# Performance work log

Hardware: AMD Instinct MI355X
Metric: run time of the kernel (lower is better)

## Reference

```python
import jax, jax.numpy as jnp
import numpy as np

N, E, B = 50000, 800000, 64
NODE_DIM, EDGE_DIM, HID, H, L = 8, 16, 128, 4, 3
C = HID // H  # head dim = 32
NUM_CLASSES, NAV_DIM = 6, 4


def _layernorm(x, g, b, eps=1e-5):
    mu = x.mean(-1, keepdims=True)
    var = ((x - mu) ** 2).mean(-1, keepdims=True)
    return (x - mu) * jax.lax.rsqrt(var + eps) * g + b


def _gat_layer(x, src, dst, e_attr, W, We, a_s, a_d, a_e, bias, n):
    # x: [N,HID]; e_attr: [Etot,EDGE_DIM]; W: [HID,HID]; We: [EDGE_DIM,HID]
    xh = (x @ W).reshape(n, H, C)                      # [N,H,C]
    eh = (e_attr @ We).reshape(-1, H, C)               # [Etot,H,C]
    a_src = (xh * a_s).sum(-1)                         # [N,H]
    a_dst = (xh * a_d).sum(-1)                         # [N,H]
    alpha = a_src[src] + a_dst[dst] + (eh * a_e).sum(-1)  # [Etot,H]
    alpha = jax.nn.leaky_relu(alpha, 0.2)
    amax = jax.ops.segment_max(alpha, dst, num_segments=n)
    alpha = jnp.exp(alpha - amax[dst])
    denom = jax.ops.segment_sum(alpha, dst, num_segments=n)
    alpha = alpha / (denom[dst] + 1e-16)               # scatter-softmax over dst
    msg = xh[src] * alpha[:, :, None]                  # [Etot,H,C]
    out = jax.ops.segment_sum(msg, dst, num_segments=n)
    return out.reshape(n, HID) + bias


def setup_inputs():
    key = jax.random.key(0)
    ks = jax.random.split(key, 32)
    s = 0.05
    inp = {
        'x': jax.random.normal(ks[0], (N, NODE_DIM), jnp.float32),
        'edge_index': jax.random.randint(ks[1], (2, E), 0, N, jnp.int64),
        'edge_attr': jax.random.normal(ks[2], (E, EDGE_DIM), jnp.float32),
        'batch': jnp.sort(jax.random.randint(ks[3], (N,), 0, B, jnp.int64)),
        'proj_W': jax.random.normal(ks[4], (NODE_DIM, HID)) * s,
        'proj_b': jnp.zeros((HID,)),
        'lin_W': jax.random.normal(ks[5], (L, HID, HID)) * s,
        'lin_edge_W': jax.random.normal(ks[6], (L, EDGE_DIM, HID)) * s,
        'att_src': jax.random.normal(ks[7], (L, H, C)) * s,
        'att_dst': jax.random.normal(ks[8], (L, H, C)) * s,
        'att_edge': jax.random.normal(ks[9], (L, H, C)) * s,
        'conv_bias': jnp.zeros((L, HID)),
        'ln_g': jnp.ones((L, HID)),
        'ln_b': jnp.zeros((L, HID)),
        'sc_W1': jax.random.normal(ks[10], (HID, HID // 2)) * s,
        'sc_b1': jnp.zeros((HID // 2,)),
        'sc_W2': jax.random.normal(ks[11], (HID // 2, NUM_CLASSES)) * s,
        'sc_b2': jnp.zeros((NUM_CLASSES,)),
        'nav_W1': jax.random.normal(ks[12], (HID, HID // 2)) * s,
        'nav_b1': jnp.zeros((HID // 2,)),
        'nav_W2': jax.random.normal(ks[13], (HID // 2, NAV_DIM)) * s,
        'nav_b2': jnp.zeros((NAV_DIM,)),
    }
    return inp


def reference(x, edge_index, edge_attr, batch, proj_W, proj_b, lin_W, lin_edge_W,
              att_src, att_dst, att_edge, conv_bias, ln_g, ln_b,
              sc_W1, sc_b1, sc_W2, sc_b2, nav_W1, nav_b1, nav_W2, nav_b2):
    n = x.shape[0]
    h = jax.nn.relu(x @ proj_W + proj_b)
    # PyG GATConv default add_self_loops=True, edge_attr fill_value='mean'
    loops = jnp.arange(n)
    src = jnp.concatenate([edge_index[0], loops])
    dst = jnp.concatenate([edge_index[1], loops])
    ea = jnp.concatenate(
        [edge_attr, jnp.broadcast_to(edge_attr.mean(0), (n, edge_attr.shape[1]))], 0)
    for l in range(L):
        res = h
        h = _gat_layer(h, src, dst, ea, lin_W[l], lin_edge_W[l],
                       att_src[l], att_dst[l], att_edge[l], conv_bias[l], n)
        h = _layernorm(h + res, ln_g[l], ln_b[l])
        h = jax.nn.relu(h)
        # dropout is identity in eval / p=0
    counts = jax.ops.segment_sum(jnp.ones((n,), h.dtype), batch, num_segments=B)
    graph = jax.ops.segment_sum(h, batch, num_segments=B) / jnp.maximum(counts, 1.0)[:, None]
    scene = jax.nn.relu(graph @ sc_W1 + sc_b1) @ sc_W2 + sc_b2
    nav = jax.nn.sigmoid(jax.nn.relu(graph @ nav_W1 + nav_b1) @ nav_W2 + nav_b2)
    return (h, scene, nav, graph)
```

## Files before the change

kernel.cpp:

```cpp
#include <hip/hip_runtime.h>
#include <hip/hip_bf16.h>

constexpr int NN   = 50000;
constexpr int NE   = 800000;
constexpr int ETOT = NE + NN;
constexpr int BGR  = 64;
constexpr int HID  = 128;
constexpr int HEADS= 4;
constexpr int CDIM = 32;
constexpr int EDIM = 16;
constexpr int NDIM = 8;
constexpr int LAYERS = 3;
constexpr int HALF = 64;
constexpr int NCLS = 6;
constexpr int NAVD = 4;

constexpr int OUT_SCENE = NN * HID;
constexpr int OUT_NAV   = OUT_SCENE + BGR*NCLS;
constexpr int OUT_GRAPH = OUT_NAV + BGR*NAVD;

__global__ void mean_ea_kernel(const float* __restrict__ ea, float* __restrict__ mean_sum) {
    __shared__ float sdata[256];
    int tid = threadIdx.x;
    float acc = 0.f;
    int stride = gridDim.x * blockDim.x;
    for (int i = blockIdx.x * blockDim.x + tid; i < NE * EDIM; i += stride)
        acc += ea[i];
    sdata[tid] = acc;
    __syncthreads();
    for (int off = 128; off >= 16; off >>= 1) {
        if (tid < off) sdata[tid] += sdata[tid + off];
        __syncthreads();
    }
    if (tid < 16) atomicAdd(&mean_sum[tid], sdata[tid]);
}

__global__ void precompute_kernel(const float* __restrict__ lin_edge_W,
                                  const float* __restrict__ att_edge,
                                  const float* __restrict__ mean_sum,
                                  float* __restrict__ w_e, float* __restrict__ mean_alpha) {
    int l = blockIdx.x;
    int t = threadIdx.x;
    __shared__ float we_s[EDIM * HEADS];
    const float* We = lin_edge_W + l * EDIM * HID;
    const float* ae = att_edge   + l * HEADS * CDIM;
    if (t < EDIM) {
        #pragma unroll
        for (int h = 0; h < HEADS; h++) {
            float s = 0.f;
            #pragma unroll
            for (int c = 0; c < CDIM; c++)
                s += We[t * HID + h * CDIM + c] * ae[h * CDIM + c];
            we_s[t * HEADS + h] = s;
            w_e[(l * EDIM + t) * HEADS + h] = s;
        }
    }
    __syncthreads();
    if (t < HEADS) {
        float s = 0.f;
        #pragma unroll
        for (int k = 0; k < EDIM; k++)
            s += (mean_sum[k] * (1.f / (float)NE)) * we_s[k * HEADS + t];
        mean_alpha[l * HEADS + t] = s;
    }
}

__global__ void proj_kernel(const float* __restrict__ x, const float* __restrict__ pW,
                            const float* __restrict__ pb, float* __restrict__ h) {
    int node = blockIdx.x;
    int t = threadIdx.x;
    __shared__ float xr[NDIM];
    if (t < NDIM) xr[t] = x[node * NDIM + t];
    __syncthreads();
    float acc = pb[t];
    #pragma unroll
    for (int k = 0; k < NDIM; k++) acc += xr[k] * pW[k * HID + t];
    h[node * HID + t] = fmaxf(acc, 0.f);
}

__launch_bounds__(256, 2)
__global__ void xh_kernel(const float* __restrict__ hin, const float* __restrict__ W,
                          const float* __restrict__ As, const float* __restrict__ Ad,
                          float* __restrict__ xh, float* __restrict__ asrc,
                          float* __restrict__ adst) {
    __shared__ float Ws[HID * HID];
    {
        const float4* Wv = (const float4*)W;
        float4* Wsv = (float4*)Ws;
        #pragma unroll
        for (int i = 0; i < (HID * HID / 4) / 256; i++)
            Wsv[i * 256 + threadIdx.x] = Wv[i * 256 + threadIdx.x];
    }
    __syncthreads();
    int t = threadIdx.x;
    int c = t & 127;
    int lane = t & 63;
    int which = __builtin_amdgcn_readfirstlane(t >> 7);
    float myAs = As[c], myAd = Ad[c];
    int head = c >> 5;

    for (int base = blockIdx.x * 4; base < NN; base += gridDim.x * 4) {
        int n0 = base + which * 2;
        int n1 = n0 + 1;
        const float* __restrict__ h0 = hin + (size_t)n0 * HID;
        const float* __restrict__ h1 = hin + (size_t)n1 * HID;
        float a0e = 0.f, a0o = 0.f, a1e = 0.f, a1o = 0.f;
        #pragma unroll 8
        for (int k = 0; k < HID; k += 2) {
            float w0 = Ws[k * HID + c];
            float w1 = Ws[(k + 1) * HID + c];
            float h0e = h0[k], h0o = h0[k + 1];
            float h1e = h1[k], h1o = h1[k + 1];
            a0e = fmaf(h0e, w0, a0e);
            a0o = fmaf(h0o, w1, a0o);
            a1e = fmaf(h1e, w0, a1e);
            a1o = fmaf(h1o, w1, a1o);
        }
        float acc0 = a0e + a0o;
        float acc1 = a1e + a1o;
        xh[(size_t)n0 * HID + c] = acc0;
        xh[(size_t)n1 * HID + c] = acc1;
        float rs0 = acc0 * myAs, rd0 = acc0 * myAd;
        float rs1 = acc1 * myAs, rd1 = acc1 * myAd;
        #pragma unroll
        for (int off = 16; off > 0; off >>= 1) {
            rs0 += __shfl_xor(rs0, off);
            rd0 += __shfl_xor(rd0, off);
            rs1 += __shfl_xor(rs1, off);
            rd1 += __shfl_xor(rd1, off);
        }
        if ((lane & 31) == 0) {
            asrc[n0 * HEADS + head] = rs0;
            adst[n0 * HEADS + head] = rd0;
            asrc[n1 * HEADS + head] = rs1;
            adst[n1 * HEADS + head] = rd1;
        }
    }
}

__global__ void hist_kernel(const int* __restrict__ ei, int* __restrict__ counts) {
    int e = blockIdx.x * blockDim.x + threadIdx.x;
    if (e >= ETOT) return;
    int d = (e < NE) ? ei[NE + e] : (e - NE);
    atomicAdd(&counts[d], 1);
}

__global__ void scan_kernel(const int* __restrict__ counts, int* __restrict__ offsets) {
    __shared__ int wsum[16];
    __shared__ int carry_s;
    int lane = threadIdx.x & 63;
    int wid  = threadIdx.x >> 6;
    if (threadIdx.x == 0) carry_s = 0;
    __syncthreads();
    for (int base = 0; base < NN; base += 1024) {
        int i = base + threadIdx.x;
        int v = (i < NN) ? counts[i] : 0;
        int x = v;
        #pragma unroll
        for (int off = 1; off < 64; off <<= 1) {
            int y = __shfl_up(x, off);
            if (lane >= off) x += y;
        }
        if (lane == 63) wsum[wid] = x;
        __syncthreads();
        if (wid == 0) {
            int w = (lane < 16) ? wsum[lane] : 0;
            #pragma unroll
            for (int off = 1; off < 16; off <<= 1) {
                int y = __shfl_up(w, off);
                if (lane >= off) w += y;
            }
            if (lane < 16) wsum[lane] = w;
        }
        __syncthreads();
        int waveoff = (wid == 0) ? 0 : wsum[wid - 1];
        int carry = carry_s;
        if (i < NN) offsets[i] = carry + waveoff + x - v;
        __syncthreads();
        if (threadIdx.x == 0) carry_s = carry + wsum[15];
        __syncthreads();
    }
}

__global__ void scatter_kernel(const int* __restrict__ ei, const int* __restrict__ offsets,
                               int* __restrict__ fill, int* __restrict__ epos,
                               int* __restrict__ src_p) {
    int e = blockIdx.x * blockDim.x + threadIdx.x;
    if (e >= ETOT) return;
    int s, d;
    if (e < NE) { s = ei[e]; d = ei[NE + e]; }
    else        { s = d = e - NE; }
    int pos = offsets[d] + atomicAdd(&fill[d], 1);
    epos[e]   = pos;
    src_p[pos] = s;
}

__global__ void eterm_kernel(const float* __restrict__ ea,
                             const float* __restrict__ w_e, const float* __restrict__ mean_alpha,
                             const int* __restrict__ epos, float* __restrict__ dst, int nl) {
    __shared__ float we_s[LAYERS * EDIM * HEADS];
    __shared__ float ma_s[LAYERS * HEADS];
    if (threadIdx.x < nl * EDIM * HEADS) we_s[threadIdx.x] = w_e[threadIdx.x];
    if (threadIdx.x < nl * HEADS) ma_s[threadIdx.x] = mean_alpha[threadIdx.x];
    __syncthreads();
    int e = blockIdx.x * blockDim.x + threadIdx.x;
    if (e >= ETOT) return;
    int pos = epos[e];
    if (e < NE) {
        float er[EDIM];
        const float4* ev = (const float4*)(ea + (size_t)e * EDIM);
        float4 v0 = ev[0], v1 = ev[1], v2 = ev[2], v3 = ev[3];
        er[0]=v0.x; er[1]=v0.y; er[2]=v0.z; er[3]=v0.w;
        er[4]=v1.x; er[5]=v1.y; er[6]=v1.z; er[7]=v1.w;
        er[8]=v2.x; er[9]=v2.y; er[10]=v2.z; er[11]=v2.w;
        er[12]=v3.x; er[13]=v3.y; er[14]=v3.z; er[15]=v3.w;
        for (int l = 0; l < nl; l++) {
            float e0 = 0.f, e1 = 0.f, e2 = 0.f, e3 = 0.f;
            const float* ws = we_s + l * EDIM * HEADS;
            #pragma unroll
            for (int k = 0; k < EDIM; k++) {
                float xv = er[k];
                e0 += xv * ws[k * HEADS + 0];
                e1 += xv * ws[k * HEADS + 1];
                e2 += xv * ws[k * HEADS + 2];
                e3 += xv * ws[k * HEADS + 3];
            }
            *(float4*)(dst + (size_t)l * ETOT * HEADS + (size_t)pos * HEADS)
                = make_float4(e0, e1, e2, e3);
        }
    } else {
        for (int l = 0; l < nl; l++) {
            *(float4*)(dst + (size_t)l * ETOT * HEADS + (size_t)pos * HEADS)
                = make_float4(ma_s[l*HEADS+0], ma_s[l*HEADS+1], ma_s[l*HEADS+2], ma_s[l*HEADS+3]);
        }
    }
}

__launch_bounds__(256)
__global__ void aggregate_kernel(const int* __restrict__ src_p, const int* __restrict__ offsets,
                                 const int* __restrict__ counts,
                                 const float* __restrict__ eterm,
                                 const float* __restrict__ asrc, const float* __restrict__ adst,
                                 const float* __restrict__ xh,
                                 const float* __restrict__ hres, const float* __restrict__ bias,
                                 const float* __restrict__ lng, const float* __restrict__ lnb,
                                 float* __restrict__ hout) {
    int wid  = threadIdx.x >> 6;
    int lane = threadIdx.x & 63;
    int node = blockIdx.x * 4 + wid;
    if (node >= NN) return;
    int start = offsets[node];
    int deg   = counts[node];
    int head  = lane >> 4;
    int c0    = lane * 2;
    float ad_h = adst[node * HEADS + head];

    float m = -1e30f, dsum = 0.f, acc0 = 0.f, acc1 = 0.f;
    int j = 0;
    for (; j + 3 < deg; j += 4) {
        int p0 = start + j, p1 = p0 + 1, p2 = p0 + 2, p3 = p0 + 3;
        int s0 = src_p[p0], s1 = src_p[p1], s2 = src_p[p2], s3 = src_p[p3];
        float a0 = asrc[s0 * HEADS + head] + ad_h + eterm[(size_t)p0 * HEADS + head];
        float a1 = asrc[s1 * HEADS + head] + ad_h + eterm[(size_t)p1 * HEADS + head];
        float a2 = asrc[s2 * HEADS + head] + ad_h + eterm[(size_t)p2 * HEADS + head];
        float a3 = asrc[s3 * HEADS + head] + ad_h + eterm[(size_t)p3 * HEADS + head];
        a0 = (a0 > 0.f) ? a0 : 0.2f * a0;
        a1 = (a1 > 0.f) ? a1 : 0.2f * a1;
        a2 = (a2 > 0.f) ? a2 : 0.2f * a2;
        a3 = (a3 > 0.f) ? a3 : 0.2f * a3;
        float2 v0 = *(const float2*)(xh + (size_t)s0 * HID + c0);
        float2 v1 = *(const float2*)(xh + (size_t)s1 * HID + c0);
        float2 v2 = *(const float2*)(xh + (size_t)s2 * HID + c0);
        float2 v3 = *(const float2*)(xh + (size_t)s3 * HID + c0);
        float mn = fmaxf(m, fmaxf(fmaxf(a0, a1), fmaxf(a2, a3)));
        float sc = __expf(m - mn);
        float q0 = __expf(a0 - mn), q1 = __expf(a1 - mn);
        float q2 = __expf(a2 - mn), q3 = __expf(a3 - mn);
        dsum = fmaf(dsum, sc, (q0 + q1) + (q2 + q3));
        acc0 = fmaf(acc0, sc, fmaf(q0, v0.x, fmaf(q1, v1.x, fmaf(q2, v2.x, q3 * v3.x))));
        acc1 = fmaf(acc1, sc, fmaf(q0, v0.y, fmaf(q1, v1.y, fmaf(q2, v2.y, q3 * v3.y))));
        m = mn;
    }
    for (; j < deg; j++) {
        int pi = start + j;
        int s0 = src_p[pi];
        float a0 = asrc[s0 * HEADS + head] + ad_h + eterm[(size_t)pi * HEADS + head];
        a0 = (a0 > 0.f) ? a0 : 0.2f * a0;
        float2 v0 = *(const float2*)(xh + (size_t)s0 * HID + c0);
        float mn = fmaxf(m, a0);
        float sc = __expf(m - mn);
        float q0 = __expf(a0 - mn);
        dsum = fmaf(dsum, sc, q0);
        acc0 = fmaf(acc0, sc, q0 * v0.x);
        acc1 = fmaf(acc1, sc, q0 * v0.y);
        m = mn;
    }
    float inv = 1.f / (dsum + 1e-16f);
    float2 r = *(const float2*)(hres + (size_t)node * HID + c0);
    float v0 = acc0 * inv + bias[c0]     + r.x;
    float v1 = acc1 * inv + bias[c0 + 1] + r.y;

    float ssum = v0 + v1;
    #pragma unroll
    for (int off = 32; off > 0; off >>= 1) ssum += __shfl_xor(ssum, off);
    float mu = ssum * (1.f / 128.f);
    float d0 = v0 - mu, d1 = v1 - mu;
    float vs = d0 * d0 + d1 * d1;
    #pragma unroll
    for (int off = 32; off > 0; off >>= 1) vs += __shfl_xor(vs, off);
    float rstd = rsqrtf(vs * (1.f / 128.f) + 1e-5f);
    float y0 = fmaxf(d0 * rstd * lng[c0]     + lnb[c0],     0.f);
    float y1 = fmaxf(d1 * rstd * lng[c0 + 1] + lnb[c0 + 1], 0.f);
    *(float2*)(hout + (size_t)node * HID + c0) = make_float2(y0, y1);
}

__launch_bounds__(512)
__global__ void head_kernel(const float* __restrict__ h, const int* __restrict__ batch,
                            const float* __restrict__ scW1, const float* __restrict__ scb1,
                            const float* __restrict__ scW2, const float* __restrict__ scb2,
                            const float* __restrict__ nvW1, const float* __restrict__ nvb1,
                            const float* __restrict__ nvW2, const float* __restrict__ nvb2,
                            float* __restrict__ out) {
    int b = blockIdx.x;
    int t = threadIdx.x;
    __shared__ float part[4][HID];
    __shared__ float gr[HID];
    __shared__ float h1[HALF];
    __shared__ float h2[HALF];
    int lo = 0, hi = NN;
    while (lo < hi) { int mid = (lo + hi) >> 1; if (batch[mid] < b) lo = mid + 1; else hi = mid; }
    int s0 = lo;
    lo = s0; hi = NN;
    while (lo < hi) { int mid = (lo + hi) >> 1; if (batch[mid] < b + 1) lo = mid + 1; else hi = mid; }
    int e0 = lo;
    int cnt = e0 - s0;

    int r  = t >> 7;
    int ch = t & 127;
    float acc = 0.f;
    for (int i = s0 + r; i < e0; i += 4) acc += h[(size_t)i * HID + ch];
    part[r][ch] = acc;
    __syncthreads();
    if (t < HID) {
        float g = (part[0][t] + part[1][t] + part[2][t] + part[3][t]) / fmaxf((float)cnt, 1.f);
        gr[t] = g;
        out[OUT_GRAPH + b * HID + t] = g;
    }
    __syncthreads();
    if (t < HALF) {
        float a = scb1[t], n = nvb1[t];
        #pragma unroll 4
        for (int k = 0; k < HID; k++) {
            float g = gr[k];
            a += g * scW1[k * HALF + t];
            n += g * nvW1[k * HALF + t];
        }
        h1[t] = fmaxf(a, 0.f);
        h2[t] = fmaxf(n, 0.f);
    }
    __syncthreads();
    if (t < NCLS) {
        float a = scb2[t];
        #pragma unroll 8
        for (int j = 0; j < HALF; j++) a += h1[j] * scW2[j * NCLS + t];
        out[OUT_SCENE + b * NCLS + t] = a;
    }
    if (t >= 64 && t < 64 + NAVD) {
        int q = t - 64;
        float a = nvb2[q];
        #pragma unroll 8
        for (int j = 0; j < HALF; j++) a += h2[j] * nvW2[j * NAVD + q];
        out[OUT_NAV + b * NAVD + q] = 1.f / (1.f + expf(-a));
    }
}

extern "C" void kernel_launch(void* const* d_in, const int* in_sizes, int n_in,
                              void* d_out, int out_size, void* d_ws, size_t ws_size,
                              hipStream_t stream) {
    const float* x        = (const float*)d_in[0];
    const int*   ei       = (const int*)  d_in[1];
    const float* ea       = (const float*)d_in[2];
    const int*   batch    = (const int*)  d_in[3];
    const float* proj_W   = (const float*)d_in[4];
    const float* proj_b   = (const float*)d_in[5];
    const float* lin_W    = (const float*)d_in[6];
    const float* lin_eW   = (const float*)d_in[7];
    const float* att_src  = (const float*)d_in[8];
    const float* att_dst  = (const float*)d_in[9];
    const float* att_edge = (const float*)d_in[10];
    const float* conv_bias= (const float*)d_in[11];
    const float* ln_g     = (const float*)d_in[12];
    const float* ln_b     = (const float*)d_in[13];
    const float* sc_W1    = (const float*)d_in[14];
    const float* sc_b1    = (const float*)d_in[15];
    const float* sc_W2    = (const float*)d_in[16];
    const float* sc_b2    = (const float*)d_in[17];
    const float* nav_W1   = (const float*)d_in[18];
    const float* nav_b1   = (const float*)d_in[19];
    const float* nav_W2   = (const float*)d_in[20];
    const float* nav_b2   = (const float*)d_in[21];
    float* out = (float*)d_out;

    char* w = (char*)d_ws;
    size_t off = 0;
    auto alloc = [&](size_t bytes) -> char* {
        char* p = w + off;
        off = (off + bytes + 255) & ~(size_t)255;
        return p;
    };
    size_t fixed = (size_t)NN*HID*4*2 + (size_t)NN*HEADS*4*2 + (size_t)NN*4*3
                 + (size_t)ETOT*4*2 + 16384;
    bool multi = (ws_size >= fixed + (size_t)LAYERS * ETOT * HEADS * 4 + 65536);
    int nl = multi ? LAYERS : 1;

    float* hA      = (float*)alloc((size_t)NN * HID * 4);
    float* xh      = (float*)alloc((size_t)NN * HID * 4);
    float* asrc    = (float*)alloc((size_t)NN * HEADS * 4);
    float* adst    = (float*)alloc((size_t)NN * HEADS * 4);
    int*   counts  = (int*)  alloc((size_t)NN * 4);
    int*   offsets = (int*)  alloc((size_t)NN * 4);
    int*   fill    = (int*)  alloc((size_t)NN * 4);
    int*   epos    = (int*)  alloc((size_t)ETOT * 4);
    int*   src_p   = (int*)  alloc((size_t)ETOT * 4);
    float* w_e     = (float*)alloc((size_t)LAYERS * EDIM * HEADS * 4);
    float* mean_s  = (float*)alloc(EDIM * 4);
    float* mean_al = (float*)alloc(LAYERS * HEADS * 4);
    float* eterm   = (float*)alloc((size_t)nl * ETOT * HEADS * 4);

    hipMemsetAsync(mean_s, 0, EDIM * 4, stream);
    hipMemsetAsync(counts, 0, (size_t)NN * 4, stream);
    hipMemsetAsync(fill,   0, (size_t)NN * 4, stream);

    mean_ea_kernel<<<256, 256, 0, stream>>>(ea, mean_s);
    precompute_kernel<<<LAYERS, 64, 0, stream>>>(lin_eW, att_edge, mean_s, w_e, mean_al);
    proj_kernel<<<NN, HID, 0, stream>>>(x, proj_W, proj_b, hA);

    int eblocks = (ETOT + 255) / 256;
    hist_kernel<<<eblocks, 256, 0, stream>>>(ei, counts);
    scan_kernel<<<1, 1024, 0, stream>>>(counts, offsets);
    scatter_kernel<<<eblocks, 256, 0, stream>>>(ei, offsets, fill, epos, src_p);
    if (multi)
        eterm_kernel<<<eblocks, 256, 0, stream>>>(ea, w_e, mean_al, epos, eterm, LAYERS);

    const float* hin = hA;
    float* hout = out;
    for (int l = 0; l < LAYERS; l++) {
        xh_kernel<<<512, 256, 0, stream>>>(hin, lin_W + (size_t)l * HID * HID,
                                           att_src + (size_t)l * HID,
                                           att_dst + (size_t)l * HID,
                                           xh, asrc, adst);
        if (!multi)
            eterm_kernel<<<eblocks, 256, 0, stream>>>(ea, w_e + (size_t)l * EDIM * HEADS,
                                                      mean_al + (size_t)l * HEADS,
                                                      epos, eterm, 1);
        const float* et_l = multi ? (eterm + (size_t)l * ETOT * HEADS) : eterm;
        aggregate_kernel<<<(NN + 3) / 4, 256, 0, stream>>>(src_p, offsets, counts,
                                                           et_l, asrc, adst, xh, hin,
                                                           conv_bias + (size_t)l * HID,
                                                           ln_g + (size_t)l * HID,
                                                           ln_b + (size_t)l * HID, hout);
        const float* tmp = hin;
        hin = hout;
        hout = (float*)tmp;
    }

    head_kernel<<<BGR, 512, 0, stream>>>(out, batch, sc_W1, sc_b1, sc_W2, sc_b2,
                                         nav_W1, nav_b1, nav_W2, nav_b2, out);
}
```

Before: 891.2 us.

## Store xh in bf16 and retile xh GEMM to 8 nodes x 4 columns per thread

New measurement: 777.0 us. 12.8% less time.

```diff
diff --git a/kernel.cpp b/kernel.cpp
--- a/kernel.cpp
+++ b/kernel.cpp
@@ -19,6 +19,9 @@
 constexpr int OUT_NAV   = OUT_SCENE + BGR*NCLS;
 constexpr int OUT_GRAPH = OUT_NAV + BGR*NAVD;
 
+#define FMA4(Wv, Sv, Cv) { (Cv).x = fmaf((Wv).x, (Sv), (Cv).x); (Cv).y = fmaf((Wv).y, (Sv), (Cv).y); \
+                           (Cv).z = fmaf((Wv).z, (Sv), (Cv).z); (Cv).w = fmaf((Wv).w, (Sv), (Cv).w); }
+
 __global__ void mean_ea_kernel(const float* __restrict__ ea, float* __restrict__ mean_sum) {
     __shared__ float sdata[256];
     int tid = threadIdx.x;
@@ -78,62 +81,77 @@
     h[node * HID + t] = fmaxf(acc, 0.f);
 }
 
-__launch_bounds__(256, 2)
-__global__ void xh_kernel(const float* __restrict__ hin, const float* __restrict__ W,
-                          const float* __restrict__ As, const float* __restrict__ Ad,
-                          float* __restrict__ xh, float* __restrict__ asrc,
-                          float* __restrict__ adst) {
+__global__ __launch_bounds__(1024)
+void xh_kernel(const float* __restrict__ hin, const float* __restrict__ W,
+               const float* __restrict__ As, const float* __restrict__ Ad,
+               __hip_bfloat16* __restrict__ xhb, float* __restrict__ asrc,
+               float* __restrict__ adst) {
     __shared__ float Ws[HID * HID];
     {
         const float4* Wv = (const float4*)W;
         float4* Wsv = (float4*)Ws;
         #pragma unroll
-        for (int i = 0; i < (HID * HID / 4) / 256; i++)
-            Wsv[i * 256 + threadIdx.x] = Wv[i * 256 + threadIdx.x];
-    }
-    __syncthreads();
+        for (int i = 0; i < 4; i++)
+            Wsv[i * 1024 + threadIdx.x] = Wv[i * 1024 + threadIdx.x];
+    }
+    __syncthreads();
+    const float4* Ws4 = (const float4*)Ws;
     int t = threadIdx.x;
-    int c = t & 127;
-    int lane = t & 63;
-    int which = __builtin_amdgcn_readfirstlane(t >> 7);
-    float myAs = As[c], myAd = Ad[c];
-    int head = c >> 5;
-
-    for (int base = blockIdx.x * 4; base < NN; base += gridDim.x * 4) {
-        int n0 = base + which * 2;
-        int n1 = n0 + 1;
-        const float* __restrict__ h0 = hin + (size_t)n0 * HID;
-        const float* __restrict__ h1 = hin + (size_t)n1 * HID;
-        float a0e = 0.f, a0o = 0.f, a1e = 0.f, a1o = 0.f;
-        #pragma unroll 8
-        for (int k = 0; k < HID; k += 2) {
-            float w0 = Ws[k * HID + c];
-            float w1 = Ws[(k + 1) * HID + c];
-            float h0e = h0[k], h0o = h0[k + 1];
-            float h1e = h1[k], h1o = h1[k + 1];
-            a0e = fmaf(h0e, w0, a0e);
-            a0o = fmaf(h0o, w1, a0o);
-            a1e = fmaf(h1e, w0, a1e);
-            a1o = fmaf(h1o, w1, a1o);
-        }
-        float acc0 = a0e + a0o;
-        float acc1 = a1e + a1o;
-        xh[(size_t)n0 * HID + c] = acc0;
-        xh[(size_t)n1 * HID + c] = acc1;
-        float rs0 = acc0 * myAs, rd0 = acc0 * myAd;
-        float rs1 = acc1 * myAs, rd1 = acc1 * myAd;
-        #pragma unroll
-        for (int off = 16; off > 0; off >>= 1) {
-            rs0 += __shfl_xor(rs0, off);
-            rd0 += __shfl_xor(rd0, off);
-            rs1 += __shfl_xor(rs1, off);
-            rd1 += __shfl_xor(rd1, off);
-        }
-        if ((lane & 31) == 0) {
-            asrc[n0 * HEADS + head] = rs0;
-            adst[n0 * HEADS + head] = rd0;
-            asrc[n1 * HEADS + head] = rs1;
-            adst[n1 * HEADS + head] = rd1;
+    int cslot = t & 31;
+    int c0 = cslot * 4;
+    int grp = t >> 5;
+    int hd = cslot >> 3;
+    float4 As4 = *(const float4*)(As + c0);
+    float4 Ad4 = *(const float4*)(Ad + c0);
+
+    for (int base = blockIdx.x * 256; base < NN; base += gridDim.x * 256) {
+        int n0 = base + grp * 8;
+        const float* hj[8];
+        #pragma unroll
+        for (int j = 0; j < 8; j++) {
+            int nj = n0 + j;
+            if (nj >= NN) nj = NN - 1;
+            hj[j] = hin + (size_t)nj * HID;
+        }
+        float4 acc[8];
+        #pragma unroll
+        for (int j = 0; j < 8; j++) acc[j] = make_float4(0.f, 0.f, 0.f, 0.f);
+
+        #pragma unroll 2
+        for (int k = 0; k < HID; k += 4) {
+            float4 w0 = Ws4[(k + 0) * 32 + cslot];
+            float4 w1 = Ws4[(k + 1) * 32 + cslot];
+            float4 w2 = Ws4[(k + 2) * 32 + cslot];
+            float4 w3 = Ws4[(k + 3) * 32 + cslot];
+            #pragma unroll
+            for (int j = 0; j < 8; j++) {
+                float4 h4 = *(const float4*)(hj[j] + k);
+                FMA4(w0, h4.x, acc[j]);
+                FMA4(w1, h4.y, acc[j]);
+                FMA4(w2, h4.z, acc[j]);
+                FMA4(w3, h4.w, acc[j]);
+            }
+        }
+
+        #pragma unroll
+        for (int j = 0; j < 8; j++) {
+            int n = n0 + j;
+            bool ok = (n < NN);
+            union { ushort4 u4; __hip_bfloat16 b[4]; } pk;
+            pk.b[0] = __float2bfloat16(acc[j].x);
+            pk.b[1] = __float2bfloat16(acc[j].y);
+            pk.b[2] = __float2bfloat16(acc[j].z);
+            pk.b[3] = __float2bfloat16(acc[j].w);
+            if (ok) *(ushort4*)(xhb + (size_t)n * HID + c0) = pk.u4;
+            float rs = acc[j].x * As4.x + acc[j].y * As4.y + acc[j].z * As4.z + acc[j].w * As4.w;
+            float rd = acc[j].x * Ad4.x + acc[j].y * Ad4.y + acc[j].z * Ad4.z + acc[j].w * Ad4.w;
+            rs += __shfl_xor(rs, 1); rd += __shfl_xor(rd, 1);
+            rs += __shfl_xor(rs, 2); rd += __shfl_xor(rd, 2);
+            rs += __shfl_xor(rs, 4); rd += __shfl_xor(rd, 4);
+            if (ok && (t & 7) == 0) {
+                asrc[n * HEADS + hd] = rs;
+                adst[n * HEADS + hd] = rd;
+            }
         }
     }
 }
@@ -241,7 +259,7 @@
                                  const int* __restrict__ counts,
                                  const float* __restrict__ eterm,
                                  const float* __restrict__ asrc, const float* __restrict__ adst,
-                                 const float* __restrict__ xh,
+                                 const __hip_bfloat16* __restrict__ xhb,
                                  const float* __restrict__ hres, const float* __restrict__ bias,
                                  const float* __restrict__ lng, const float* __restrict__ lnb,
                                  float* __restrict__ hout) {
@@ -268,17 +286,21 @@
         a1 = (a1 > 0.f) ? a1 : 0.2f * a1;
         a2 = (a2 > 0.f) ? a2 : 0.2f * a2;
         a3 = (a3 > 0.f) ? a3 : 0.2f * a3;
-        float2 v0 = *(const float2*)(xh + (size_t)s0 * HID + c0);
-        float2 v1 = *(const float2*)(xh + (size_t)s1 * HID + c0);
-        float2 v2 = *(const float2*)(xh + (size_t)s2 * HID + c0);
-        float2 v3 = *(const float2*)(xh + (size_t)s3 * HID + c0);
+        __hip_bfloat162 b0 = *(const __hip_bfloat162*)(xhb + (size_t)s0 * HID + c0);
+        __hip_bfloat162 b1 = *(const __hip_bfloat162*)(xhb + (size_t)s1 * HID + c0);
+        __hip_bfloat162 b2 = *(const __hip_bfloat162*)(xhb + (size_t)s2 * HID + c0);
+        __hip_bfloat162 b3 = *(const __hip_bfloat162*)(xhb + (size_t)s3 * HID + c0);
         float mn = fmaxf(m, fmaxf(fmaxf(a0, a1), fmaxf(a2, a3)));
         float sc = __expf(m - mn);
         float q0 = __expf(a0 - mn), q1 = __expf(a1 - mn);
         float q2 = __expf(a2 - mn), q3 = __expf(a3 - mn);
         dsum = fmaf(dsum, sc, (q0 + q1) + (q2 + q3));
-        acc0 = fmaf(acc0, sc, fmaf(q0, v0.x, fmaf(q1, v1.x, fmaf(q2, v2.x, q3 * v3.x))));
-        acc1 = fmaf(acc1, sc, fmaf(q0, v0.y, fmaf(q1, v1.y, fmaf(q2, v2.y, q3 * v3.y))));
+        acc0 = fmaf(acc0, sc, fmaf(q0, __bfloat162float(b0.x),
+                     fmaf(q1, __bfloat162float(b1.x),
+                     fmaf(q2, __bfloat162float(b2.x), q3 * __bfloat162float(b3.x)))));
+        acc1 = fmaf(acc1, sc, fmaf(q0, __bfloat162float(b0.y),
+                     fmaf(q1, __bfloat162float(b1.y),
+                     fmaf(q2, __bfloat162float(b2.y), q3 * __bfloat162float(b3.y)))));
         m = mn;
     }
     for (; j < deg; j++) {
@@ -286,13 +308,13 @@
         int s0 = src_p[pi];
         float a0 = asrc[s0 * HEADS + head] + ad_h + eterm[(size_t)pi * HEADS + head];
         a0 = (a0 > 0.f) ? a0 : 0.2f * a0;
-        float2 v0 = *(const float2*)(xh + (size_t)s0 * HID + c0);
+        __hip_bfloat162 b0 = *(const __hip_bfloat162*)(xhb + (size_t)s0 * HID + c0);
         float mn = fmaxf(m, a0);
         float sc = __expf(m - mn);
         float q0 = __expf(a0 - mn);
         dsum = fmaf(dsum, sc, q0);
-        acc0 = fmaf(acc0, sc, q0 * v0.x);
-        acc1 = fmaf(acc1, sc, q0 * v0.y);
+        acc0 = fmaf(acc0, sc, q0 * __bfloat162float(b0.x));
+        acc1 = fmaf(acc1, sc, q0 * __bfloat162float(b0.y));
         m = mn;
     }
     float inv = 1.f / (dsum + 1e-16f);
@@ -408,13 +430,13 @@
         off = (off + bytes + 255) & ~(size_t)255;
         return p;
     };
-    size_t fixed = (size_t)NN*HID*4*2 + (size_t)NN*HEADS*4*2 + (size_t)NN*4*3
+    size_t fixed = (size_t)NN*HID*4 + (size_t)NN*HID*2 + (size_t)NN*HEADS*4*2 + (size_t)NN*4*3
                  + (size_t)ETOT*4*2 + 16384;
     bool multi = (ws_size >= fixed + (size_t)LAYERS * ETOT * HEADS * 4 + 65536);
     int nl = multi ? LAYERS : 1;
 
-    float* hA      = (float*)alloc((size_t)NN * HID * 4);
-    float* xh      = (float*)alloc((size_t)NN * HID * 4);
+    float* hA              = (float*)alloc((size_t)NN * HID * 4);
+    __hip_bfloat16* xhb    = (__hip_bfloat16*)alloc((size_t)NN * HID * 2);
     float* asrc    = (float*)alloc((size_t)NN * HEADS * 4);
     float* adst    = (float*)alloc((size_t)NN * HEADS * 4);
     int*   counts  = (int*)  alloc((size_t)NN * 4);
@@ -427,9 +449,9 @@
     float* mean_al = (float*)alloc(LAYERS * HEADS * 4);
     float* eterm   = (float*)alloc((size_t)nl * ETOT * HEADS * 4);
 
-    hipMemsetAsync(mean_s, 0, EDIM * 4, stream);
-    hipMemsetAsync(counts, 0, (size_t)NN * 4, stream);
-    hipMemsetAsync(fill,   0, (size_t)NN * 4, stream);
+    (void)hipMemsetAsync(mean_s, 0, EDIM * 4, stream);
+    (void)hipMemsetAsync(counts, 0, (size_t)NN * 4, stream);
+    (void)hipMemsetAsync(fill,   0, (size_t)NN * 4, stream);
 
     mean_ea_kernel<<<256, 256, 0, stream>>>(ea, mean_s);
     precompute_kernel<<<LAYERS, 64, 0, stream>>>(lin_eW, att_edge, mean_s, w_e, mean_al);
@@ -442,20 +464,21 @@
     if (multi)
         eterm_kernel<<<eblocks, 256, 0, stream>>>(ea, w_e, mean_al, epos, eterm, LAYERS);
 
+    int xblocks = (NN + 255) / 256;
     const float* hin = hA;
     float* hout = out;
     for (int l = 0; l < LAYERS; l++) {
-        xh_kernel<<<512, 256, 0, stream>>>(hin, lin_W + (size_t)l * HID * HID,
-                                           att_src + (size_t)l * HID,
-                                           att_dst + (size_t)l * HID,
-                                           xh, asrc, adst);
+        xh_kernel<<<xblocks, 1024, 0, stream>>>(hin, lin_W + (size_t)l * HID * HID,
+                                                att_src + (size_t)l * HID,
+                                                att_dst + (size_t)l * HID,
+                                                xhb, asrc, adst);
         if (!multi)
             eterm_kernel<<<eblocks, 256, 0, stream>>>(ea, w_e + (size_t)l * EDIM * HEADS,
                                                       mean_al + (size_t)l * HEADS,
                                                       epos, eterm, 1);
         const float* et_l = multi ? (eterm + (size_t)l * ETOT * HEADS) : eterm;
         aggregate_kernel<<<(NN + 3) / 4, 256, 0, stream>>>(src_p, offsets, counts,
-                                                           et_l, asrc, adst, xh, hin,
+                                                           et_l, asrc, adst, xhb, hin,
                                                            conv_bias + (size_t)l * HID,
                                                            ln_g + (size_t)l * HID,
                                                            ln_b + (size_t)l * HID, hout);
```
